# Kernel tuning notes

Measured on AMD Instinct MI355X. Metric: run time of the kernel, lower is better.

The kernel has to match this reference:

```python
import jax, jax.numpy as jnp
import numpy as np
import math

D_MODEL, N_LEVELS, N_HEADS, N_POINTS = 256, 4, 8, 4
D_HEAD = D_MODEL // N_HEADS
SPATIAL = np.array([[128, 128], [64, 64], [32, 32], [16, 16]], dtype=np.int32)  # (H_l, W_l)
LEN_IN = int((SPATIAL[:, 0] * SPATIAL[:, 1]).sum())  # 21760
N_BATCH, LEN_Q = 8, 1000


def _offset_bias():
    # torch _reset_parameters grid_init
    thetas = np.arange(N_HEADS, dtype=np.float32) * (2.0 * math.pi / N_HEADS)
    grid = np.stack([np.cos(thetas), np.sin(thetas)], -1)
    grid = grid / np.abs(grid).max(-1, keepdims=True)
    grid = np.tile(grid.reshape(N_HEADS, 1, 1, 2), (1, N_LEVELS, N_POINTS, 1))
    for i in range(N_POINTS):
        grid[:, :, i, :] *= i + 1
    return jnp.asarray(grid.reshape(-1), dtype=jnp.float32)


def setup_inputs() -> dict:
    key = jax.random.key(0)
    ks = jax.random.split(key, 8)
    s = 1.0 / math.sqrt(D_MODEL)
    return {
        "query": jax.random.normal(ks[0], (N_BATCH, LEN_Q, D_MODEL), jnp.float32),
        "reference_points": jax.random.uniform(ks[1], (N_BATCH, LEN_Q, N_LEVELS, 2), jnp.float32),
        "input_flatten": jax.random.normal(ks[2], (N_BATCH, LEN_IN, D_MODEL), jnp.float32),
        "input_spatial_shapes": jnp.asarray(SPATIAL),
        "input_level_start_index": jnp.asarray(np.concatenate([[0], np.cumsum(SPATIAL[:, 0] * SPATIAL[:, 1])[:-1]]).astype(np.int32)),
        # params (W stored as (in, out); y = x @ W + b)
        "W_off": jax.random.normal(ks[3], (D_MODEL, N_HEADS * N_LEVELS * N_POINTS * 2), jnp.float32) * 0.01,
        "b_off": _offset_bias(),
        "W_attn": jax.random.normal(ks[4], (D_MODEL, N_HEADS * N_LEVELS * N_POINTS), jnp.float32) * 0.02,
        "b_attn": jnp.zeros((N_HEADS * N_LEVELS * N_POINTS,), jnp.float32),
        "W_val": jax.random.normal(ks[5], (D_MODEL, D_MODEL), jnp.float32) * s,
        "b_val": jnp.zeros((D_MODEL,), jnp.float32),
        "W_out": jax.random.normal(ks[6], (D_MODEL, D_MODEL), jnp.float32) * s,
        "b_out": jnp.zeros((D_MODEL,), jnp.float32),
    }


def _bilinear_sample(v, x, y, H, W):
    # v: (N, nH, H*W, dH); x, y: (N, nH, Lq, nP) in pixel coords (grid_sample align_corners=False, zeros padding)
    Nb, nH, Lq, nP = x.shape
    x0 = jnp.floor(x); y0 = jnp.floor(y)
    wx1 = x - x0; wy1 = y - y0
    x0i = x0.astype(jnp.int32); y0i = y0.astype(jnp.int32)
    out = jnp.zeros((Nb, nH, Lq, nP, v.shape[-1]), v.dtype)
    for dy, wy in ((0, 1.0 - wy1), (1, wy1)):
        for dx, wx in ((0, 1.0 - wx1), (1, wx1)):
            ix = x0i + dx; iy = y0i + dy
            valid = (ix >= 0) & (ix < W) & (iy >= 0) & (iy < H)
            idx = (jnp.clip(iy, 0, H - 1) * W + jnp.clip(ix, 0, W - 1)).reshape(Nb, nH, Lq * nP, 1)
            g = jnp.take_along_axis(v, idx, axis=2).reshape(Nb, nH, Lq, nP, -1)
            out = out + g * (wy * wx * valid.astype(v.dtype))[..., None]
    return out


def reference(query, reference_points, input_flatten, input_spatial_shapes, input_level_start_index,
              W_off, b_off, W_attn, b_attn, W_val, b_val, W_out, b_out):
    shapes = np.asarray(input_spatial_shapes)          # static metadata
    starts = np.asarray(input_level_start_index)
    Nb, Lq, _ = query.shape

    value = input_flatten @ W_val + b_val              # (N, Lin, C)
    value = value.reshape(Nb, -1, N_HEADS, D_HEAD).transpose(0, 2, 1, 3)  # (N, nH, Lin, dH)

    offsets = (query @ W_off + b_off).reshape(Nb, Lq, N_HEADS, N_LEVELS, N_POINTS, 2)
    attn = jax.nn.softmax((query @ W_attn + b_attn).reshape(Nb, Lq, N_HEADS, N_LEVELS * N_POINTS), axis=-1)
    attn = attn.reshape(Nb, Lq, N_HEADS, N_LEVELS, N_POINTS)

    # normalizer is (W_l, H_l) per level; locations in [0,1]
    normalizer = jnp.asarray(np.stack([shapes[:, 1], shapes[:, 0]], -1), jnp.float32)
    loc = reference_points[:, :, None, :, None, :] + offsets / normalizer[None, None, None, :, None, :]

    out = jnp.zeros((Nb, N_HEADS, Lq, D_HEAD), value.dtype)
    for l in range(N_LEVELS):
        H, W = int(shapes[l, 0]), int(shapes[l, 1])
        s = int(starts[l])
        v_l = value[:, :, s:s + H * W]                             # (N, nH, HW, dH)
        loc_l = loc[:, :, :, l].transpose(0, 2, 1, 3, 4)           # (N, nH, Lq, nP, 2)
        x = loc_l[..., 0] * W - 0.5
        y = loc_l[..., 1] * H - 0.5
        sampled = _bilinear_sample(v_l, x, y, H, W)                # (N, nH, Lq, nP, dH)
        a_l = attn[:, :, :, l].transpose(0, 2, 1, 3)               # (N, nH, Lq, nP)
        out = out + jnp.einsum('nhqpd,nhqp->nhqd', sampled, a_l)

    out = out.transpose(0, 2, 1, 3).reshape(Nb, Lq, D_MODEL)
    return out @ W_out + b_out
```

## Files before the change

### kernel.cpp

```cpp
#include <hip/hip_runtime.h>
#include <hip/hip_bf16.h>

#define D_MODEL 256
#define N_HEADS 8
#define D_HEAD 32
#define N_LEVELS 4
#define N_POINTS 4
#define LEN_IN 21760
#define N_BATCH 8
#define LEN_Q 1000

typedef __attribute__((ext_vector_type(8))) short short8;
typedef __attribute__((ext_vector_type(4))) float f32x4;

typedef const __attribute__((address_space(1))) void* gp1;
typedef __attribute__((address_space(3))) void* lp3;

__device__ __forceinline__ unsigned short f2bf(float f) {
    unsigned int u = __float_as_uint(f);
    u += 0x7FFFu + ((u >> 16) & 1u);
    return (unsigned short)(u >> 16);
}
__device__ __forceinline__ float bf2f(unsigned short s) {
    return __uint_as_float(((unsigned int)s) << 16);
}

__global__ __launch_bounds__(256) void prep_kernel(
    const float* __restrict__ Wv, const float* __restrict__ Wo,
    const float* __restrict__ Wa, const float* __restrict__ Wu,
    const float* __restrict__ boff, const float* __restrict__ battn,
    unsigned short* __restrict__ WtVp, unsigned short* __restrict__ WtC,
    unsigned short* __restrict__ WtO, float* __restrict__ bcat)
{
    int idx = blockIdx.x * 256 + threadIdx.x;
    if (idx < 65536) {
        int j = idx & 7, lane = (idx >> 3) & 63, nf = (idx >> 9) & 15, ks = idx >> 13;
        int col = nf * 16 + (lane & 15);
        int k = ks * 32 + (lane >> 4) * 8 + j;
        WtVp[idx] = f2bf(Wv[k * 256 + col]);
    } else if (idx < 65536 + 98304) {
        int j = idx - 65536;
        int n = j >> 8, k = j & 255;
        float s = (n < 256) ? Wo[k * 256 + n] : Wa[k * 128 + (n - 256)];
        WtC[j] = f2bf(s);
    } else if (idx < 65536 + 98304 + 65536) {
        int j = idx - (65536 + 98304);
        int n = j >> 8, k = j & 255;
        WtO[j] = f2bf(Wu[k * 256 + n]);
    } else if (idx < 65536 + 98304 + 65536 + 384) {
        int j = idx - (65536 + 98304 + 65536);
        bcat[j] = (j < 256) ? boff[j] : battn[j - 256];
    }
}

__global__ __launch_bounds__(256) void gemm_value(
    const float* __restrict__ A,
    const unsigned short* __restrict__ Bp,
    const float* __restrict__ bias,
    unsigned short* __restrict__ C)
{
    __shared__ float lds[2][2048];

    const int tid = threadIdx.x;
    const int wave = tid >> 6, lane = tid & 63;
    const int lhi = lane >> 4, llo = lane & 15;
    const int mBase = blockIdx.x * 64;

    const int soff = tid * 16;
    const int r0 = soff >> 7, cb0 = soff & 127;
    const size_t g0 = (size_t)r0 * 1024 + (size_t)(cb0 ^ ((r0 & 7) << 4));
    const size_t g1 = g0 + (size_t)32 * 1024;

    const char* Ab = (const char*)(A + (size_t)mBase * 256);
    const int dsto = soff >> 2;

    f32x4 acc[4][4];
#pragma unroll
    for (int mf = 0; mf < 4; ++mf)
#pragma unroll
        for (int n = 0; n < 4; ++n)
            acc[mf][n] = (f32x4){0.f, 0.f, 0.f, 0.f};

    {
        float* dst0 = &lds[0][dsto];
        __builtin_amdgcn_global_load_lds((gp1)(const void*)(Ab + g0),
                                         (lp3)dst0, 16, 0, 0);
        __builtin_amdgcn_global_load_lds((gp1)(const void*)(Ab + g1),
                                         (lp3)(dst0 + 1024), 16, 0, 0);
    }

#pragma unroll
    for (int kt = 0; kt < 8; ++kt) {
        const int cur = kt & 1;

        short8 b[4];
#pragma unroll
        for (int n = 0; n < 4; ++n)
            b[n] = *reinterpret_cast<const short8*>(
                Bp + ((size_t)(kt * 16 + wave * 4 + n) * 64 + lane) * 8);

        if (kt < 7) {
            const size_t off = (size_t)(kt + 1) * 128;
            float* dst0 = &lds[cur ^ 1][dsto];
            __builtin_amdgcn_global_load_lds((gp1)(const void*)(Ab + off + g0),
                                             (lp3)dst0, 16, 0, 0);
            __builtin_amdgcn_global_load_lds((gp1)(const void*)(Ab + off + g1),
                                             (lp3)(dst0 + 1024), 16, 0, 0);
        }

        __builtin_amdgcn_sched_barrier(0);
        if (kt < 7) asm volatile("s_waitcnt vmcnt(2)" ::: "memory");
        else        asm volatile("s_waitcnt vmcnt(0)" ::: "memory");
        __builtin_amdgcn_sched_barrier(0);
        __builtin_amdgcn_s_barrier();
        __builtin_amdgcn_sched_barrier(0);

        short8 af[4];
#pragma unroll
        for (int mf = 0; mf < 4; ++mf) {
            const int row = mf * 16 + llo;
            const int sz = (llo & 7) << 4;
            const char* base = (const char*)&lds[cur][0] + row * 128;
            f32x4 flo = *reinterpret_cast<const f32x4*>(base + ((lhi * 32) ^ sz));
            f32x4 fhi = *reinterpret_cast<const f32x4*>(base + ((lhi * 32 + 16) ^ sz));
            short8 t;
            t[0] = (short)f2bf(flo[0]); t[1] = (short)f2bf(flo[1]);
            t[2] = (short)f2bf(flo[2]); t[3] = (short)f2bf(flo[3]);
            t[4] = (short)f2bf(fhi[0]); t[5] = (short)f2bf(fhi[1]);
            t[6] = (short)f2bf(fhi[2]); t[7] = (short)f2bf(fhi[3]);
            af[mf] = t;
        }

#pragma unroll
        for (int mf = 0; mf < 4; ++mf)
#pragma unroll
            for (int n = 0; n < 4; ++n)
                acc[mf][n] = __builtin_amdgcn_mfma_f32_16x16x32_bf16(
                    af[mf], b[n], acc[mf][n], 0, 0, 0);

        __builtin_amdgcn_sched_barrier(0);
        __builtin_amdgcn_s_barrier();
        __builtin_amdgcn_sched_barrier(0);
    }

#pragma unroll
    for (int mf = 0; mf < 4; ++mf) {
        const int row0 = mBase + mf * 16 + lhi * 4;
#pragma unroll
        for (int n = 0; n < 4; ++n) {
            const int col = wave * 64 + n * 16 + llo;
            const float bb = bias[col];
#pragma unroll
            for (int r = 0; r < 4; ++r)
                C[(size_t)(row0 + r) * 256 + col] = f2bf(acc[mf][n][r] + bb);
        }
    }
}

template<int NF, bool ABF16, bool OBF16>
__global__ __launch_bounds__(256) void gemm_k256(
    const void* __restrict__ Av, const unsigned short* __restrict__ Wt,
    const float* __restrict__ bias, void* __restrict__ Cv)
{
    const int wave = threadIdx.x >> 6;
    const int lane = threadIdx.x & 63;
    const int lhi = lane >> 4, llo = lane & 15;
    const int mBase = blockIdx.x * 16;
    const int colBase = wave * (NF * 16);
    const int N = NF * 64;

    f32x4 acc[NF];
#pragma unroll
    for (int n = 0; n < NF; ++n)
        acc[n] = (f32x4){0.f, 0.f, 0.f, 0.f};

#pragma unroll
    for (int ks = 0; ks < 8; ++ks) {
        const int kk = ks * 32 + lhi * 8;
        short8 a;
        if (ABF16) {
            a = *reinterpret_cast<const short8*>(
                (const unsigned short*)Av + (size_t)(mBase + llo) * 256 + kk);
        } else {
            const float* ap = (const float*)Av + (size_t)(mBase + llo) * 256 + kk;
            f32x4 f0 = *reinterpret_cast<const f32x4*>(ap);
            f32x4 f1 = *reinterpret_cast<const f32x4*>(ap + 4);
            short8 t;
            t[0] = (short)f2bf(f0[0]); t[1] = (short)f2bf(f0[1]);
            t[2] = (short)f2bf(f0[2]); t[3] = (short)f2bf(f0[3]);
            t[4] = (short)f2bf(f1[0]); t[5] = (short)f2bf(f1[1]);
            t[6] = (short)f2bf(f1[2]); t[7] = (short)f2bf(f1[3]);
            a = t;
        }
        short8 b[NF];
#pragma unroll
        for (int n = 0; n < NF; ++n) {
            const unsigned short* bp =
                Wt + (size_t)(colBase + n * 16 + llo) * 256 + kk;
            b[n] = *reinterpret_cast<const short8*>(bp);
        }
#pragma unroll
        for (int n = 0; n < NF; ++n)
            acc[n] = __builtin_amdgcn_mfma_f32_16x16x32_bf16(
                a, b[n], acc[n], 0, 0, 0);
    }

    const int row0 = mBase + lhi * 4;
#pragma unroll
    for (int n = 0; n < NF; ++n) {
        const int col = colBase + n * 16 + llo;
        const float bb = bias[col];
#pragma unroll
        for (int r = 0; r < 4; ++r) {
            float v = acc[n][r] + bb;
            size_t idx = (size_t)(row0 + r) * N + col;
            if (OBF16) ((unsigned short*)Cv)[idx] = f2bf(v);
            else       ((float*)Cv)[idx] = v;
        }
    }
}

__global__ __launch_bounds__(512) void ms_sample_kernel(
    const unsigned short* __restrict__ value,
    const float* __restrict__ proj,
    const float* __restrict__ refp,
    unsigned short* __restrict__ out_h)
{
    const int bid = blockIdx.x;
    const int b = bid & 7;
    const int q = bid >> 3;
    const int bq = b * LEN_Q + q;

    const int h = threadIdx.x >> 6;
    const int lane = threadIdx.x & 63;
    const int g = (lane >> 4) & 3;
    const int ld = lane & 15;

    const float* prow = proj + (size_t)bq * 384;

    float lg = prow[256 + h * 16 + ld];
    float mx = lg;
    mx = fmaxf(mx, __shfl_xor(mx, 1, 16));
    mx = fmaxf(mx, __shfl_xor(mx, 2, 16));
    mx = fmaxf(mx, __shfl_xor(mx, 4, 16));
    mx = fmaxf(mx, __shfl_xor(mx, 8, 16));
    float e = __expf(lg - mx);
    float den = e;
    den += __shfl_xor(den, 1, 16);
    den += __shfl_xor(den, 2, 16);
    den += __shfl_xor(den, 4, 16);
    den += __shfl_xor(den, 8, 16);
    const float w = e / den;
    float myw[4];
#pragma unroll
    for (int l = 0; l < 4; ++l)
        myw[l] = __shfl(w, l * 4 + g, 16);

    const unsigned short* vbase =
        value + (size_t)b * LEN_IN * 256 + h * 32 + 2 * ld;

    unsigned int vraw[4][4];
    float wgt[4][4];

#pragma unroll
    for (int l = 0; l < 4; ++l) {
        const int Wl = 128 >> l;
        const int STL[4] = {0, 16384, 20480, 21504};
        const int st = STL[l];
        const int s = l * 4 + g;

        const float dx = prow[h * 32 + 2 * s];
        const float dy = prow[h * 32 + 2 * s + 1];
        const float rx = refp[((size_t)bq * 4 + l) * 2 + 0];
        const float ry = refp[((size_t)bq * 4 + l) * 2 + 1];

        const float x = rx * (float)Wl + dx - 0.5f;
        const float y = ry * (float)Wl + dy - 0.5f;
        const float x0f = floorf(x), y0f = floorf(y);
        const int x0 = (int)x0f, y0 = (int)y0f;
        const float wx1 = x - x0f, wy1 = y - y0f;
        const float wx0 = 1.f - wx1, wy0 = 1.f - wy1;
        const float ws = myw[l];

        const int x0c = min(max(x0, 0), Wl - 1);
        const int x1c = min(max(x0 + 1, 0), Wl - 1);
        const int y0c = min(max(y0, 0), Wl - 1);
        const int y1c = min(max(y0 + 1, 0), Wl - 1);
        const float fx0 = (x0 >= 0 && x0 < Wl) ? 1.f : 0.f;
        const float fx1 = (x0 + 1 >= 0 && x0 + 1 < Wl) ? 1.f : 0.f;
        const float fy0 = (y0 >= 0 && y0 < Wl) ? 1.f : 0.f;
        const float fy1 = (y0 + 1 >= 0 && y0 + 1 < Wl) ? 1.f : 0.f;

        const int r0 = st + y0c * Wl, r1 = st + y1c * Wl;
        vraw[l][0] = *reinterpret_cast<const unsigned int*>(vbase + (size_t)(r0 + x0c) * 256);
        vraw[l][1] = *reinterpret_cast<const unsigned int*>(vbase + (size_t)(r0 + x1c) * 256);
        vraw[l][2] = *reinterpret_cast<const unsigned int*>(vbase + (size_t)(r1 + x0c) * 256);
        vraw[l][3] = *reinterpret_cast<const unsigned int*>(vbase + (size_t)(r1 + x1c) * 256);
        wgt[l][0] = ws * wy0 * wx0 * fy0 * fx0;
        wgt[l][1] = ws * wy0 * wx1 * fy0 * fx1;
        wgt[l][2] = ws * wy1 * wx0 * fy1 * fx0;
        wgt[l][3] = ws * wy1 * wx1 * fy1 * fx1;
    }

    float ax = 0.f, ay = 0.f;
#pragma unroll
    for (int l = 0; l < 4; ++l)
#pragma unroll
        for (int n = 0; n < 4; ++n) {
            const unsigned int v = vraw[l][n];
            const float wv = wgt[l][n];
            ax += wv * bf2f((unsigned short)(v & 0xFFFFu));
            ay += wv * bf2f((unsigned short)(v >> 16));
        }

    ax += __shfl_xor(ax, 16, 64);
    ay += __shfl_xor(ay, 16, 64);
    ax += __shfl_xor(ax, 32, 64);
    ay += __shfl_xor(ay, 32, 64);

    if (g == 0) {
        unsigned int o = (unsigned int)f2bf(ax) | ((unsigned int)f2bf(ay) << 16);
        *reinterpret_cast<unsigned int*>(
            out_h + (size_t)bq * 256 + h * 32 + 2 * ld) = o;
    }
}

extern "C" void kernel_launch(void* const* d_in, const int* in_sizes, int n_in,
                              void* d_out, int out_size, void* d_ws, size_t ws_size,
                              hipStream_t stream)
{
    const float* query  = (const float*)d_in[0];
    const float* refp   = (const float*)d_in[1];
    const float* inpf   = (const float*)d_in[2];
    const float* W_off  = (const float*)d_in[5];
    const float* b_off  = (const float*)d_in[6];
    const float* W_attn = (const float*)d_in[7];
    const float* b_attn = (const float*)d_in[8];
    const float* W_val  = (const float*)d_in[9];
    const float* b_val  = (const float*)d_in[10];
    const float* W_out  = (const float*)d_in[11];
    const float* b_out  = (const float*)d_in[12];

    char* ws = (char*)d_ws;
    unsigned short* value = (unsigned short*)(ws);
    float*          proj  = (float*)(ws + 89128960);
    unsigned short* out_h = (unsigned short*)(ws + 89128960 + 12288000);
    unsigned short* WtVp  = (unsigned short*)(ws + 109608960);
    unsigned short* WtC   = (unsigned short*)(ws + 109740032);
    unsigned short* WtO   = (unsigned short*)(ws + 109936640);
    float*          bcat  = (float*)(ws + 110067712);

    prep_kernel<<<898, 256, 0, stream>>>(W_val, W_off, W_attn, W_out,
                                         b_off, b_attn, WtVp, WtC, WtO, bcat);

    gemm_value<<<(N_BATCH * LEN_IN) / 64, 256, 0, stream>>>(
        inpf, WtVp, b_val, value);

    gemm_k256<6, false, false><<<(N_BATCH * LEN_Q) / 16, 256, 0, stream>>>(
        query, WtC, bcat, (void*)proj);

    ms_sample_kernel<<<N_BATCH * LEN_Q, 512, 0, stream>>>(
        value, proj, refp, out_h);

    gemm_k256<4, true, false><<<(N_BATCH * LEN_Q) / 16, 256, 0, stream>>>(
        out_h, WtO, b_out, d_out);
}
```

Before: 136.8 us.

## Remap sampling threads so each lane loads 16-byte value chunks per sample point

```diff
diff --git a/kernel.cpp b/kernel.cpp
--- a/kernel.cpp
+++ b/kernel.cpp
@@ -12,6 +12,7 @@
 
 typedef __attribute__((ext_vector_type(8))) short short8;
 typedef __attribute__((ext_vector_type(4))) float f32x4;
+typedef __attribute__((ext_vector_type(4))) unsigned int u32x4;
 
 typedef const __attribute__((address_space(1))) void* gp1;
 typedef __attribute__((address_space(3))) void* lp3;
@@ -233,12 +234,13 @@
 
     const int h = threadIdx.x >> 6;
     const int lane = threadIdx.x & 63;
-    const int g = (lane >> 4) & 3;
-    const int ld = lane & 15;
+    const int task = lane >> 2;
+    const int l = task >> 2;
+    const int qd = lane & 3;
 
     const float* prow = proj + (size_t)bq * 384;
 
-    float lg = prow[256 + h * 16 + ld];
+    float lg = prow[256 + h * 16 + (lane & 15)];
     float mx = lg;
     mx = fmaxf(mx, __shfl_xor(mx, 1, 16));
     mx = fmaxf(mx, __shfl_xor(mx, 2, 16));
@@ -250,78 +252,82 @@
     den += __shfl_xor(den, 2, 16);
     den += __shfl_xor(den, 4, 16);
     den += __shfl_xor(den, 8, 16);
-    const float w = e / den;
-    float myw[4];
-#pragma unroll
-    for (int l = 0; l < 4; ++l)
-        myw[l] = __shfl(w, l * 4 + g, 16);
-
-    const unsigned short* vbase =
-        value + (size_t)b * LEN_IN * 256 + h * 32 + 2 * ld;
-
-    unsigned int vraw[4][4];
-    float wgt[4][4];
-
-#pragma unroll
-    for (int l = 0; l < 4; ++l) {
-        const int Wl = 128 >> l;
-        const int STL[4] = {0, 16384, 20480, 21504};
-        const int st = STL[l];
-        const int s = l * 4 + g;
-
-        const float dx = prow[h * 32 + 2 * s];
-        const float dy = prow[h * 32 + 2 * s + 1];
-        const float rx = refp[((size_t)bq * 4 + l) * 2 + 0];
-        const float ry = refp[((size_t)bq * 4 + l) * 2 + 1];
-
-        const float x = rx * (float)Wl + dx - 0.5f;
-        const float y = ry * (float)Wl + dy - 0.5f;
-        const float x0f = floorf(x), y0f = floorf(y);
-        const int x0 = (int)x0f, y0 = (int)y0f;
-        const float wx1 = x - x0f, wy1 = y - y0f;
-        const float wx0 = 1.f - wx1, wy0 = 1.f - wy1;
-        const float ws = myw[l];
-
-        const int x0c = min(max(x0, 0), Wl - 1);
-        const int x1c = min(max(x0 + 1, 0), Wl - 1);
-        const int y0c = min(max(y0, 0), Wl - 1);
-        const int y1c = min(max(y0 + 1, 0), Wl - 1);
-        const float fx0 = (x0 >= 0 && x0 < Wl) ? 1.f : 0.f;
-        const float fx1 = (x0 + 1 >= 0 && x0 + 1 < Wl) ? 1.f : 0.f;
-        const float fy0 = (y0 >= 0 && y0 < Wl) ? 1.f : 0.f;
-        const float fy1 = (y0 + 1 >= 0 && y0 + 1 < Wl) ? 1.f : 0.f;
-
-        const int r0 = st + y0c * Wl, r1 = st + y1c * Wl;
-        vraw[l][0] = *reinterpret_cast<const unsigned int*>(vbase + (size_t)(r0 + x0c) * 256);
-        vraw[l][1] = *reinterpret_cast<const unsigned int*>(vbase + (size_t)(r0 + x1c) * 256);
-        vraw[l][2] = *reinterpret_cast<const unsigned int*>(vbase + (size_t)(r1 + x0c) * 256);
-        vraw[l][3] = *reinterpret_cast<const unsigned int*>(vbase + (size_t)(r1 + x1c) * 256);
-        wgt[l][0] = ws * wy0 * wx0 * fy0 * fx0;
-        wgt[l][1] = ws * wy0 * wx1 * fy0 * fx1;
-        wgt[l][2] = ws * wy1 * wx0 * fy1 * fx0;
-        wgt[l][3] = ws * wy1 * wx1 * fy1 * fx1;
-    }
-
-    float ax = 0.f, ay = 0.f;
-#pragma unroll
-    for (int l = 0; l < 4; ++l)
-#pragma unroll
-        for (int n = 0; n < 4; ++n) {
-            const unsigned int v = vraw[l][n];
-            const float wv = wgt[l][n];
-            ax += wv * bf2f((unsigned short)(v & 0xFFFFu));
-            ay += wv * bf2f((unsigned short)(v >> 16));
-        }
-
-    ax += __shfl_xor(ax, 16, 64);
-    ay += __shfl_xor(ay, 16, 64);
-    ax += __shfl_xor(ax, 32, 64);
-    ay += __shfl_xor(ay, 32, 64);
-
-    if (g == 0) {
-        unsigned int o = (unsigned int)f2bf(ax) | ((unsigned int)f2bf(ay) << 16);
-        *reinterpret_cast<unsigned int*>(
-            out_h + (size_t)bq * 256 + h * 32 + 2 * ld) = o;
+    const float wsm = e / den;
+    const float ws = __shfl(wsm, task, 16);
+
+    const int Wl = 128 >> l;
+    const int st = (65536 - (65536 >> (l << 1))) / 3;
+
+    const float dx = prow[h * 32 + 2 * task];
+    const float dy = prow[h * 32 + 2 * task + 1];
+    const float rx = refp[((size_t)bq * 4 + l) * 2 + 0];
+    const float ry = refp[((size_t)bq * 4 + l) * 2 + 1];
+
+    const float Wlf = (float)Wl;
+    const float x = rx * Wlf + dx - 0.5f;
+    const float y = ry * Wlf + dy - 0.5f;
+    const float x0f = floorf(x), y0f = floorf(y);
+    const int x0 = (int)x0f, y0 = (int)y0f;
+    const float wx1 = x - x0f, wy1 = y - y0f;
+    const float wx0 = 1.f - wx1, wy0 = 1.f - wy1;
+
+    const int x0c = min(max(x0, 0), Wl - 1);
+    const int x1c = min(max(x0 + 1, 0), Wl - 1);
+    const int y0c = min(max(y0, 0), Wl - 1);
+    const int y1c = min(max(y0 + 1, 0), Wl - 1);
+    const float fx0 = (x0 >= 0 && x0 < Wl) ? 1.f : 0.f;
+    const float fx1 = (x0 + 1 >= 0 && x0 + 1 < Wl) ? 1.f : 0.f;
+    const float fy0 = (y0 >= 0 && y0 < Wl) ? 1.f : 0.f;
+    const float fy1 = (y0 + 1 >= 0 && y0 + 1 < Wl) ? 1.f : 0.f;
+
+    const int rr0 = st + y0c * Wl, rr1 = st + y1c * Wl;
+    const int r00 = rr0 + x0c, r01 = rr0 + x1c;
+    const int r10 = rr1 + x0c, r11 = rr1 + x1c;
+
+    float wgt[4];
+    wgt[0] = ws * wy0 * wx0 * fy0 * fx0;
+    wgt[1] = ws * wy0 * wx1 * fy0 * fx1;
+    wgt[2] = ws * wy1 * wx0 * fy1 * fx0;
+    wgt[3] = ws * wy1 * wx1 * fy1 * fx1;
+
+    const char* vb = (const char*)value + (size_t)b * LEN_IN * 512
+                   + h * 64 + qd * 16;
+    u32x4 v0 = *reinterpret_cast<const u32x4*>(vb + (size_t)r00 * 512);
+    u32x4 v1 = *reinterpret_cast<const u32x4*>(vb + (size_t)r01 * 512);
+    u32x4 v2 = *reinterpret_cast<const u32x4*>(vb + (size_t)r10 * 512);
+    u32x4 v3 = *reinterpret_cast<const u32x4*>(vb + (size_t)r11 * 512);
+
+    float acc[8];
+#pragma unroll
+    for (int j = 0; j < 8; ++j) acc[j] = 0.f;
+#pragma unroll
+    for (int n = 0; n < 4; ++n) {
+        const u32x4 v = (n == 0) ? v0 : (n == 1) ? v1 : (n == 2) ? v2 : v3;
+        const float wn = wgt[n];
+#pragma unroll
+        for (int j = 0; j < 4; ++j) {
+            const unsigned int u = v[j];
+            acc[2 * j]     += wn * bf2f((unsigned short)(u & 0xFFFFu));
+            acc[2 * j + 1] += wn * bf2f((unsigned short)(u >> 16));
+        }
+    }
+
+#pragma unroll
+    for (int j = 0; j < 8; ++j) {
+        acc[j] += __shfl_xor(acc[j], 4, 64);
+        acc[j] += __shfl_xor(acc[j], 8, 64);
+        acc[j] += __shfl_xor(acc[j], 16, 64);
+        acc[j] += __shfl_xor(acc[j], 32, 64);
+    }
+
+    if (task == 0) {
+        u32x4 o;
+#pragma unroll
+        for (int j = 0; j < 4; ++j)
+            o[j] = (unsigned int)f2bf(acc[2 * j]) |
+                   ((unsigned int)f2bf(acc[2 * j + 1]) << 16);
+        *reinterpret_cast<u32x4*>(
+            out_h + (size_t)bq * 256 + h * 32 + qd * 8) = o;
     }
 }
 
```

Result: faster. 132.2 us (-3.4%).
